# Kernel optimization log

Hardware: AMD Instinct MI355X
Metric: run time of the kernel (lower is better)

Reference implementation:

```python
import jax, jax.numpy as jnp
import numpy as np

D_K = 128

def setup_inputs() -> dict:
    key = jax.random.key(0)
    k1, k2, k3 = jax.random.split(key, 3)
    q = jax.random.normal(k1, (8192, D_K), dtype=jnp.float32)
    k = jax.random.normal(k2, (8192, D_K), dtype=jnp.float32)
    v = jax.random.normal(k3, (8192, D_K), dtype=jnp.float32)
    return {"q": q, "k": k, "v": v}

def reference(q, k, v):
    # scores: [S_q, S_k]
    scores = jnp.einsum('qd,kd->qk', q, k) / jnp.sqrt(jnp.float32(D_K))
    attn = jax.nn.softmax(scores, axis=-1)  # softmax over keys (torch default last dim)
    return jnp.einsum('qk,kd->qd', attn, v)
```

## Files before the change

### kernel.cpp

```cpp
#include <hip/hip_runtime.h>
#include <math.h>


typedef _Float16 f16x8 __attribute__((ext_vector_type(8)));
typedef float    f32x16 __attribute__((ext_vector_type(16)));

constexpr int S_LEN = 8192;
constexpr int D_K   = 128;
constexpr int NSLICE = 8;
constexpr int ITERS2 = (S_LEN / NSLICE) / 64;

constexpr size_t WS_L_OFF = 0;
constexpr size_t KV_OFF   = 262144;
constexpr size_t PART_OFF = KV_OFF + (size_t)256 * 16384;
constexpr size_t WS_NEED  = PART_OFF + (size_t)7 * S_LEN * D_K * 4;

#define CSCALE (0.08838834764831845f * 1.44269504088896340736f)

union UH8 { _Float16 h[8]; uint4 q; f16x8 v; };
union UF4 { unsigned u[4]; uint4 q; f16x8 v; };

__device__ inline void async16(const uint4* g, uint4* l) {
  __builtin_amdgcn_global_load_lds(
      (const __attribute__((address_space(1))) unsigned int*)g,
      (__attribute__((address_space(3))) unsigned int*)l, 16, 0, 0);
}

template <bool ZOUT>
__global__ __launch_bounds__(512) void attn_prep(const float* __restrict__ K,
                                                 const float* __restrict__ V,
                                                 float* __restrict__ out,
                                                 char* __restrict__ ws) {
  const int t = blockIdx.x * 512 + threadIdx.x;
  uint4* KVg = (uint4*)(ws + KV_OFF);
  if (t < 131072) {
    int kt = t >> 9, idx = t & 511;
    int lane = idx & 63, s = idx >> 6;
    int key = kt * 32 + (lane & 31);
    int d0  = s * 16 + (lane >> 5) * 8;
    const float4* src = (const float4*)(K + (size_t)key * D_K + d0);
    float4 a = src[0], b = src[1];
    float f[8] = {a.x, a.y, a.z, a.w, b.x, b.y, b.z, b.w};
    UH8 h;
    #pragma unroll
    for (int j = 0; j < 8; ++j) h.h[j] = (_Float16)f[j];
    KVg[(size_t)kt * 1024 + idx] = h.q;
  } else if (t < 262144) {
    int g = t - 131072;
    int kt = g >> 9, idx = g & 511;
    int lane = idx & 63, c = (idx >> 6) & 3, kstep = idx >> 8;
    int d  = c * 32 + (lane & 31);
    int kb = kt * 32 + kstep * 16 + (lane >> 5) * 8;
    UH8 h;
    #pragma unroll
    for (int j = 0; j < 8; ++j) h.h[j] = (_Float16)V[(size_t)(kb + j) * D_K + d];
    KVg[(size_t)kt * 1024 + 512 + idx] = h.q;
  } else if (ZOUT && t < 327680) {
    int i = t - 262144;
    float4 z = make_float4(0.f, 0.f, 0.f, 0.f);
    float4* o4 = (float4*)out;
    #pragma unroll
    for (int j = 0; j < 4; ++j) o4[(size_t)i * 4 + j] = z;
  } else if (ZOUT && t < 329728) {
    int i = t - 327680;
    ((float4*)(ws + WS_L_OFF))[i] = make_float4(0.f, 0.f, 0.f, 0.f);
  }
}

template <bool PARTIAL>
__global__ __launch_bounds__(256, 2)
void attn_main(const float* __restrict__ Qg, float* __restrict__ out,
               char* __restrict__ ws) {
  __shared__ uint4 KV[2][2048];

  const int tid   = threadIdx.x;
  const int wave  = tid >> 6;
  const int lane  = tid & 63;
  const int lrow  = lane & 31;
  const int lhalf = lane >> 5;

  const int blk = blockIdx.x;
  const int ks  = blk & 7;
  const int qb  = blk >> 3;
  const int qw  = qb * 128 + wave * 32;

  float* ws_l = (float*)(ws + WS_L_OFF);

  f16x8 qf[8];
  {
    const int q = qw + lrow;
    #pragma unroll
    for (int s = 0; s < 8; ++s) {
      const float4* src = (const float4*)(Qg + (size_t)q * D_K + s * 16 + lhalf * 8);
      float4 a = src[0], b = src[1];
      float f[8] = {a.x, a.y, a.z, a.w, b.x, b.y, b.z, b.w};
      UH8 h;
      #pragma unroll
      for (int j = 0; j < 8; ++j) h.h[j] = (_Float16)(f[j] * CSCALE);
      qf[s] = h.v;
    }
  }

  f32x16 O0{}, O1{}, O2{}, O3{};
  float lsum = 0.f;

  const uint4* KVg = (const uint4*)(ws + KV_OFF);

  {
    const size_t base = (size_t)ks * 32768;
    #pragma unroll
    for (int i = 0; i < 8; ++i)
      async16(KVg + base + i * 256 + tid, &KV[0][i * 256 + tid]);
  }

  for (int it = 0; it < ITERS2; ++it) {
    const int buf = it & 1;
    __syncthreads();

    if (it + 1 < ITERS2) {
      const size_t base = (size_t)ks * 32768 + (size_t)(it + 1) * 2048;
      #pragma unroll
      for (int i = 0; i < 8; ++i)
        async16(KVg + base + i * 256 + tid, &KV[buf ^ 1][i * 256 + tid]);
    }

    const uint4* sub0 = &KV[buf][0];
    const uint4* sub1 = &KV[buf][1024];

    f32x16 Sa0{}, Sb0{}, Sa1{}, Sb1{};
    #pragma unroll
    for (int s = 0; s < 4; ++s) {
      f16x8 ka0 = __builtin_bit_cast(f16x8, sub0[(2 * s    ) * 64 + lane]);
      f16x8 kb0 = __builtin_bit_cast(f16x8, sub0[(2 * s + 1) * 64 + lane]);
      Sa0 = __builtin_amdgcn_mfma_f32_32x32x16_f16(ka0, qf[2 * s    ], Sa0, 0, 0, 0);
      Sb0 = __builtin_amdgcn_mfma_f32_32x32x16_f16(kb0, qf[2 * s + 1], Sb0, 0, 0, 0);
    }
    #pragma unroll
    for (int s = 0; s < 4; ++s) {
      f16x8 ka1 = __builtin_bit_cast(f16x8, sub1[(2 * s    ) * 64 + lane]);
      f16x8 kb1 = __builtin_bit_cast(f16x8, sub1[(2 * s + 1) * 64 + lane]);
      Sa1 = __builtin_amdgcn_mfma_f32_32x32x16_f16(ka1, qf[2 * s    ], Sa1, 0, 0, 0);
      Sb1 = __builtin_amdgcn_mfma_f32_32x32x16_f16(kb1, qf[2 * s + 1], Sb1, 0, 0, 0);
    }

    UF4 A00, A01;
    {
      unsigned pk[8];
      #pragma unroll
      for (int i = 0; i < 8; ++i) {
        float p0 = __builtin_amdgcn_exp2f(Sa0[2 * i]     + Sb0[2 * i]);
        float p1 = __builtin_amdgcn_exp2f(Sa0[2 * i + 1] + Sb0[2 * i + 1]);
        lsum += p0 + p1;
        pk[i] = __builtin_bit_cast(unsigned, __builtin_amdgcn_cvt_pkrtz(p0, p1));
      }
      unsigned s0 = __shfl_xor(pk[0], 32), s1 = __shfl_xor(pk[1], 32);
      unsigned s2 = __shfl_xor(pk[2], 32), s3 = __shfl_xor(pk[3], 32);
      unsigned s4 = __shfl_xor(pk[4], 32), s5 = __shfl_xor(pk[5], 32);
      unsigned s6 = __shfl_xor(pk[6], 32), s7 = __shfl_xor(pk[7], 32);
      A00.u[0] = lhalf ? s2 : pk[0];
      A00.u[1] = lhalf ? s3 : pk[1];
      A00.u[2] = lhalf ? pk[2] : s0;
      A00.u[3] = lhalf ? pk[3] : s1;
      A01.u[0] = lhalf ? s6 : pk[4];
      A01.u[1] = lhalf ? s7 : pk[5];
      A01.u[2] = lhalf ? pk[6] : s4;
      A01.u[3] = lhalf ? pk[7] : s5;
    }

    #pragma unroll
    for (int kstep = 0; kstep < 2; ++kstep) {
      f16x8 pf = kstep ? A01.v : A00.v;
      f16x8 v0 = __builtin_bit_cast(f16x8, sub0[512 + kstep * 256 +   0 + lane]);
      f16x8 v1 = __builtin_bit_cast(f16x8, sub0[512 + kstep * 256 +  64 + lane]);
      f16x8 v2 = __builtin_bit_cast(f16x8, sub0[512 + kstep * 256 + 128 + lane]);
      f16x8 v3 = __builtin_bit_cast(f16x8, sub0[512 + kstep * 256 + 192 + lane]);
      O0 = __builtin_amdgcn_mfma_f32_32x32x16_f16(pf, v0, O0, 0, 0, 0);
      O1 = __builtin_amdgcn_mfma_f32_32x32x16_f16(pf, v1, O1, 0, 0, 0);
      O2 = __builtin_amdgcn_mfma_f32_32x32x16_f16(pf, v2, O2, 0, 0, 0);
      O3 = __builtin_amdgcn_mfma_f32_32x32x16_f16(pf, v3, O3, 0, 0, 0);
    }

    UF4 A10, A11;
    {
      unsigned pk[8];
      #pragma unroll
      for (int i = 0; i < 8; ++i) {
        float p0 = __builtin_amdgcn_exp2f(Sa1[2 * i]     + Sb1[2 * i]);
        float p1 = __builtin_amdgcn_exp2f(Sa1[2 * i + 1] + Sb1[2 * i + 1]);
        lsum += p0 + p1;
        pk[i] = __builtin_bit_cast(unsigned, __builtin_amdgcn_cvt_pkrtz(p0, p1));
      }
      unsigned s0 = __shfl_xor(pk[0], 32), s1 = __shfl_xor(pk[1], 32);
      unsigned s2 = __shfl_xor(pk[2], 32), s3 = __shfl_xor(pk[3], 32);
      unsigned s4 = __shfl_xor(pk[4], 32), s5 = __shfl_xor(pk[5], 32);
      unsigned s6 = __shfl_xor(pk[6], 32), s7 = __shfl_xor(pk[7], 32);
      A10.u[0] = lhalf ? s2 : pk[0];
      A10.u[1] = lhalf ? s3 : pk[1];
      A10.u[2] = lhalf ? pk[2] : s0;
      A10.u[3] = lhalf ? pk[3] : s1;
      A11.u[0] = lhalf ? s6 : pk[4];
      A11.u[1] = lhalf ? s7 : pk[5];
      A11.u[2] = lhalf ? pk[6] : s4;
      A11.u[3] = lhalf ? pk[7] : s5;
    }

    #pragma unroll
    for (int kstep = 0; kstep < 2; ++kstep) {
      f16x8 pf = kstep ? A11.v : A10.v;
      f16x8 v0 = __builtin_bit_cast(f16x8, sub1[512 + kstep * 256 +   0 + lane]);
      f16x8 v1 = __builtin_bit_cast(f16x8, sub1[512 + kstep * 256 +  64 + lane]);
      f16x8 v2 = __builtin_bit_cast(f16x8, sub1[512 + kstep * 256 + 128 + lane]);
      f16x8 v3 = __builtin_bit_cast(f16x8, sub1[512 + kstep * 256 + 192 + lane]);
      O0 = __builtin_amdgcn_mfma_f32_32x32x16_f16(pf, v0, O0, 0, 0, 0);
      O1 = __builtin_amdgcn_mfma_f32_32x32x16_f16(pf, v1, O1, 0, 0, 0);
      O2 = __builtin_amdgcn_mfma_f32_32x32x16_f16(pf, v2, O2, 0, 0, 0);
      O3 = __builtin_amdgcn_mfma_f32_32x32x16_f16(pf, v3, O3, 0, 0, 0);
    }
  }

  lsum += __shfl_xor(lsum, 32);

  if (PARTIAL) {
    if (lhalf == 0) ws_l[ks * S_LEN + qw + lrow] = lsum;
    float* obase = (ks == 0) ? out
                 : (float*)(ws + PART_OFF) + (size_t)(ks - 1) * S_LEN * D_K;
    #pragma unroll
    for (int r = 0; r < 16; ++r) {
      int row = (r & 3) + 8 * (r >> 2) + 4 * lhalf;
      float* dst = obase + (size_t)(qw + row) * D_K + lrow;
      dst[ 0] = O0[r];
      dst[32] = O1[r];
      dst[64] = O2[r];
      dst[96] = O3[r];
    }
  } else {
    if (lhalf == 0) atomicAdd(ws_l + qw + lrow, lsum);
    #pragma unroll
    for (int r = 0; r < 16; ++r) {
      int row = (r & 3) + 8 * (r >> 2) + 4 * lhalf;
      float* dst = out + (size_t)(qw + row) * D_K + lrow;
      atomicAdd(dst +  0, O0[r]);
      atomicAdd(dst + 32, O1[r]);
      atomicAdd(dst + 64, O2[r]);
      atomicAdd(dst + 96, O3[r]);
    }
  }
}

__global__ __launch_bounds__(256) void attn_norm(float* __restrict__ out,
                                                 const float* __restrict__ lpart,
                                                 const float* __restrict__ opart,
                                                 int nparts) {
  int i = blockIdx.x * 256 + threadIdx.x;
  int q = i >> 5;
  float4* o4 = (float4*)out;
  float4 acc = o4[i];
  float l = lpart[q];
  for (int s = 1; s <= nparts; ++s) {
    float4 p = ((const float4*)opart)[(size_t)(s - 1) * 262144 + i];
    acc.x += p.x; acc.y += p.y; acc.z += p.z; acc.w += p.w;
    l += lpart[s * S_LEN + q];
  }
  float inv = 1.0f / l;
  acc.x *= inv; acc.y *= inv; acc.z *= inv; acc.w *= inv;
  o4[i] = acc;
}

extern "C" void kernel_launch(void* const* d_in, const int* in_sizes, int n_in,
                              void* d_out, int out_size, void* d_ws, size_t ws_size,
                              hipStream_t stream) {
  const float* q = (const float*)d_in[0];
  const float* k = (const float*)d_in[1];
  const float* v = (const float*)d_in[2];
  float* out = (float*)d_out;
  char* ws = (char*)d_ws;

  if (ws_size >= WS_NEED) {
    attn_prep<false><<<dim3(512), dim3(512), 0, stream>>>(k, v, out, ws);
    attn_main<true><<<dim3(512), dim3(256), 0, stream>>>(q, out, ws);
    attn_norm<<<dim3(1024), dim3(256), 0, stream>>>(
        out, (const float*)(ws + WS_L_OFF), (const float*)(ws + PART_OFF), 7);
  } else {
    attn_prep<true><<<dim3(645), dim3(512), 0, stream>>>(k, v, out, ws);
    attn_main<false><<<dim3(512), dim3(256), 0, stream>>>(q, out, ws);
    attn_norm<<<dim3(1024), dim3(256), 0, stream>>>(
        out, (const float*)(ws + WS_L_OFF), (const float*)(ws + PART_OFF), 0);
  }
}
```

Baseline: 115.5 us.

## Process two 32-row query tiles per wave to reuse K/V register fragments

Each wave now handles 64 query rows (two 32-row tiles) instead of 32, so blocks shrink to 2 waves of 128 threads. K and V fragments are loaded from LDS once per sub-tile and reused for both query tiles, halving LDS read traffic per unit of MFMA work. The cost is roughly double the accumulator and Q registers per wave, plus fewer waves per block (launch bounds 128,1), which may cut occupancy and latency hiding.

```diff
diff --git a/kernel.cpp b/kernel.cpp
--- a/kernel.cpp
+++ b/kernel.cpp
@@ -67,8 +67,44 @@
   }
 }
 
+__device__ inline void softmax32(const f32x16& Sa, const f32x16& Sb, int lhalf,
+                                 float& lsum, UF4& A0, UF4& A1) {
+  unsigned pk[8];
+  #pragma unroll
+  for (int i = 0; i < 8; ++i) {
+    float p0 = __builtin_amdgcn_exp2f(Sa[2 * i]     + Sb[2 * i]);
+    float p1 = __builtin_amdgcn_exp2f(Sa[2 * i + 1] + Sb[2 * i + 1]);
+    lsum += p0 + p1;
+    pk[i] = __builtin_bit_cast(unsigned, __builtin_amdgcn_cvt_pkrtz(p0, p1));
+  }
+  unsigned s0 = __shfl_xor(pk[0], 32), s1 = __shfl_xor(pk[1], 32);
+  unsigned s2 = __shfl_xor(pk[2], 32), s3 = __shfl_xor(pk[3], 32);
+  unsigned s4 = __shfl_xor(pk[4], 32), s5 = __shfl_xor(pk[5], 32);
+  unsigned s6 = __shfl_xor(pk[6], 32), s7 = __shfl_xor(pk[7], 32);
+  A0.u[0] = lhalf ? s2 : pk[0];
+  A0.u[1] = lhalf ? s3 : pk[1];
+  A0.u[2] = lhalf ? pk[2] : s0;
+  A0.u[3] = lhalf ? pk[3] : s1;
+  A1.u[0] = lhalf ? s6 : pk[4];
+  A1.u[1] = lhalf ? s7 : pk[5];
+  A1.u[2] = lhalf ? pk[6] : s4;
+  A1.u[3] = lhalf ? pk[7] : s5;
+}
+
+__device__ inline void pv8(const UF4& A0, const UF4& A1, const f16x8* vf,
+                           f32x16* O) {
+  #pragma unroll
+  for (int kstep = 0; kstep < 2; ++kstep) {
+    f16x8 pf = kstep ? A1.v : A0.v;
+    O[0] = __builtin_amdgcn_mfma_f32_32x32x16_f16(pf, vf[kstep * 4 + 0], O[0], 0, 0, 0);
+    O[1] = __builtin_amdgcn_mfma_f32_32x32x16_f16(pf, vf[kstep * 4 + 1], O[1], 0, 0, 0);
+    O[2] = __builtin_amdgcn_mfma_f32_32x32x16_f16(pf, vf[kstep * 4 + 2], O[2], 0, 0, 0);
+    O[3] = __builtin_amdgcn_mfma_f32_32x32x16_f16(pf, vf[kstep * 4 + 3], O[3], 0, 0, 0);
+  }
+}
+
 template <bool PARTIAL>
-__global__ __launch_bounds__(256, 2)
+__global__ __launch_bounds__(128, 1)
 void attn_main(const float* __restrict__ Qg, float* __restrict__ out,
                char* __restrict__ ws) {
   __shared__ uint4 KV[2][2048];
@@ -82,13 +118,14 @@
   const int blk = blockIdx.x;
   const int ks  = blk & 7;
   const int qb  = blk >> 3;
-  const int qw  = qb * 128 + wave * 32;
+  const int qw  = qb * 128 + wave * 64;
 
   float* ws_l = (float*)(ws + WS_L_OFF);
 
-  f16x8 qf[8];
-  {
-    const int q = qw + lrow;
+  f16x8 qf[2][8];
+  #pragma unroll
+  for (int qt = 0; qt < 2; ++qt) {
+    const int q = qw + qt * 32 + lrow;
     #pragma unroll
     for (int s = 0; s < 8; ++s) {
       const float4* src = (const float4*)(Qg + (size_t)q * D_K + s * 16 + lhalf * 8);
@@ -97,20 +134,21 @@
       UH8 h;
       #pragma unroll
       for (int j = 0; j < 8; ++j) h.h[j] = (_Float16)(f[j] * CSCALE);
-      qf[s] = h.v;
-    }
-  }
-
-  f32x16 O0{}, O1{}, O2{}, O3{};
-  float lsum = 0.f;
+      qf[qt][s] = h.v;
+    }
+  }
+
+  f32x16 O0[4] = {f32x16{}, f32x16{}, f32x16{}, f32x16{}};
+  f32x16 O1[4] = {f32x16{}, f32x16{}, f32x16{}, f32x16{}};
+  float ls0 = 0.f, ls1 = 0.f;
 
   const uint4* KVg = (const uint4*)(ws + KV_OFF);
 
   {
     const size_t base = (size_t)ks * 32768;
     #pragma unroll
-    for (int i = 0; i < 8; ++i)
-      async16(KVg + base + i * 256 + tid, &KV[0][i * 256 + tid]);
+    for (int i = 0; i < 16; ++i)
+      async16(KVg + base + i * 128 + tid, &KV[0][i * 128 + tid]);
   }
 
   for (int it = 0; it < ITERS2; ++it) {
@@ -120,129 +158,88 @@
     if (it + 1 < ITERS2) {
       const size_t base = (size_t)ks * 32768 + (size_t)(it + 1) * 2048;
       #pragma unroll
+      for (int i = 0; i < 16; ++i)
+        async16(KVg + base + i * 128 + tid, &KV[buf ^ 1][i * 128 + tid]);
+    }
+
+    #pragma unroll
+    for (int st = 0; st < 2; ++st) {
+      const uint4* sub = &KV[buf][st * 1024];
+
+      f16x8 kf[8];
+      #pragma unroll
+      for (int s = 0; s < 8; ++s)
+        kf[s] = __builtin_bit_cast(f16x8, sub[s * 64 + lane]);
+
+      f32x16 Sa0{}, Sb0{}, Sa1{}, Sb1{};
+      #pragma unroll
+      for (int s = 0; s < 4; ++s) {
+        Sa0 = __builtin_amdgcn_mfma_f32_32x32x16_f16(kf[2 * s    ], qf[0][2 * s    ], Sa0, 0, 0, 0);
+        Sb0 = __builtin_amdgcn_mfma_f32_32x32x16_f16(kf[2 * s + 1], qf[0][2 * s + 1], Sb0, 0, 0, 0);
+      }
+      #pragma unroll
+      for (int s = 0; s < 4; ++s) {
+        Sa1 = __builtin_amdgcn_mfma_f32_32x32x16_f16(kf[2 * s    ], qf[1][2 * s    ], Sa1, 0, 0, 0);
+        Sb1 = __builtin_amdgcn_mfma_f32_32x32x16_f16(kf[2 * s + 1], qf[1][2 * s + 1], Sb1, 0, 0, 0);
+      }
+
+      f16x8 vf[8];
+      #pragma unroll
       for (int i = 0; i < 8; ++i)
-        async16(KVg + base + i * 256 + tid, &KV[buf ^ 1][i * 256 + tid]);
-    }
-
-    const uint4* sub0 = &KV[buf][0];
-    const uint4* sub1 = &KV[buf][1024];
-
-    f32x16 Sa0{}, Sb0{}, Sa1{}, Sb1{};
-    #pragma unroll
-    for (int s = 0; s < 4; ++s) {
-      f16x8 ka0 = __builtin_bit_cast(f16x8, sub0[(2 * s    ) * 64 + lane]);
-      f16x8 kb0 = __builtin_bit_cast(f16x8, sub0[(2 * s + 1) * 64 + lane]);
-      Sa0 = __builtin_amdgcn_mfma_f32_32x32x16_f16(ka0, qf[2 * s    ], Sa0, 0, 0, 0);
-      Sb0 = __builtin_amdgcn_mfma_f32_32x32x16_f16(kb0, qf[2 * s + 1], Sb0, 0, 0, 0);
-    }
-    #pragma unroll
-    for (int s = 0; s < 4; ++s) {
-      f16x8 ka1 = __builtin_bit_cast(f16x8, sub1[(2 * s    ) * 64 + lane]);
-      f16x8 kb1 = __builtin_bit_cast(f16x8, sub1[(2 * s + 1) * 64 + lane]);
-      Sa1 = __builtin_amdgcn_mfma_f32_32x32x16_f16(ka1, qf[2 * s    ], Sa1, 0, 0, 0);
-      Sb1 = __builtin_amdgcn_mfma_f32_32x32x16_f16(kb1, qf[2 * s + 1], Sb1, 0, 0, 0);
-    }
-
-    UF4 A00, A01;
-    {
-      unsigned pk[8];
-      #pragma unroll
-      for (int i = 0; i < 8; ++i) {
-        float p0 = __builtin_amdgcn_exp2f(Sa0[2 * i]     + Sb0[2 * i]);
-        float p1 = __builtin_amdgcn_exp2f(Sa0[2 * i + 1] + Sb0[2 * i + 1]);
-        lsum += p0 + p1;
-        pk[i] = __builtin_bit_cast(unsigned, __builtin_amdgcn_cvt_pkrtz(p0, p1));
-      }
-      unsigned s0 = __shfl_xor(pk[0], 32), s1 = __shfl_xor(pk[1], 32);
-      unsigned s2 = __shfl_xor(pk[2], 32), s3 = __shfl_xor(pk[3], 32);
-      unsigned s4 = __shfl_xor(pk[4], 32), s5 = __shfl_xor(pk[5], 32);
-      unsigned s6 = __shfl_xor(pk[6], 32), s7 = __shfl_xor(pk[7], 32);
-      A00.u[0] = lhalf ? s2 : pk[0];
-      A00.u[1] = lhalf ? s3 : pk[1];
-      A00.u[2] = lhalf ? pk[2] : s0;
-      A00.u[3] = lhalf ? pk[3] : s1;
-      A01.u[0] = lhalf ? s6 : pk[4];
-      A01.u[1] = lhalf ? s7 : pk[5];
-      A01.u[2] = lhalf ? pk[6] : s4;
-      A01.u[3] = lhalf ? pk[7] : s5;
-    }
-
-    #pragma unroll
-    for (int kstep = 0; kstep < 2; ++kstep) {
-      f16x8 pf = kstep ? A01.v : A00.v;
-      f16x8 v0 = __builtin_bit_cast(f16x8, sub0[512 + kstep * 256 +   0 + lane]);
-      f16x8 v1 = __builtin_bit_cast(f16x8, sub0[512 + kstep * 256 +  64 + lane]);
-      f16x8 v2 = __builtin_bit_cast(f16x8, sub0[512 + kstep * 256 + 128 + lane]);
-      f16x8 v3 = __builtin_bit_cast(f16x8, sub0[512 + kstep * 256 + 192 + lane]);
-      O0 = __builtin_amdgcn_mfma_f32_32x32x16_f16(pf, v0, O0, 0, 0, 0);
-      O1 = __builtin_amdgcn_mfma_f32_32x32x16_f16(pf, v1, O1, 0, 0, 0);
-      O2 = __builtin_amdgcn_mfma_f32_32x32x16_f16(pf, v2, O2, 0, 0, 0);
-      O3 = __builtin_amdgcn_mfma_f32_32x32x16_f16(pf, v3, O3, 0, 0, 0);
-    }
-
-    UF4 A10, A11;
-    {
-      unsigned pk[8];
-      #pragma unroll
-      for (int i = 0; i < 8; ++i) {
-        float p0 = __builtin_amdgcn_exp2f(Sa1[2 * i]     + Sb1[2 * i]);
-        float p1 = __builtin_amdgcn_exp2f(Sa1[2 * i + 1] + Sb1[2 * i + 1]);
-        lsum += p0 + p1;
-        pk[i] = __builtin_bit_cast(unsigned, __builtin_amdgcn_cvt_pkrtz(p0, p1));
-      }
-      unsigned s0 = __shfl_xor(pk[0], 32), s1 = __shfl_xor(pk[1], 32);
-      unsigned s2 = __shfl_xor(pk[2], 32), s3 = __shfl_xor(pk[3], 32);
-      unsigned s4 = __shfl_xor(pk[4], 32), s5 = __shfl_xor(pk[5], 32);
-      unsigned s6 = __shfl_xor(pk[6], 32), s7 = __shfl_xor(pk[7], 32);
-      A10.u[0] = lhalf ? s2 : pk[0];
-      A10.u[1] = lhalf ? s3 : pk[1];
-      A10.u[2] = lhalf ? pk[2] : s0;
-      A10.u[3] = lhalf ? pk[3] : s1;
-      A11.u[0] = lhalf ? s6 : pk[4];
-      A11.u[1] = lhalf ? s7 : pk[5];
-      A11.u[2] = lhalf ? pk[6] : s4;
-      A11.u[3] = lhalf ? pk[7] : s5;
-    }
-
-    #pragma unroll
-    for (int kstep = 0; kstep < 2; ++kstep) {
-      f16x8 pf = kstep ? A11.v : A10.v;
-      f16x8 v0 = __builtin_bit_cast(f16x8, sub1[512 + kstep * 256 +   0 + lane]);
-      f16x8 v1 = __builtin_bit_cast(f16x8, sub1[512 + kstep * 256 +  64 + lane]);
-      f16x8 v2 = __builtin_bit_cast(f16x8, sub1[512 + kstep * 256 + 128 + lane]);
-      f16x8 v3 = __builtin_bit_cast(f16x8, sub1[512 + kstep * 256 + 192 + lane]);
-      O0 = __builtin_amdgcn_mfma_f32_32x32x16_f16(pf, v0, O0, 0, 0, 0);
-      O1 = __builtin_amdgcn_mfma_f32_32x32x16_f16(pf, v1, O1, 0, 0, 0);
-      O2 = __builtin_amdgcn_mfma_f32_32x32x16_f16(pf, v2, O2, 0, 0, 0);
-      O3 = __builtin_amdgcn_mfma_f32_32x32x16_f16(pf, v3, O3, 0, 0, 0);
-    }
-  }
-
-  lsum += __shfl_xor(lsum, 32);
+        vf[i] = __builtin_bit_cast(f16x8, sub[512 + i * 64 + lane]);
+
+      UF4 A00, A01;
+      softmax32(Sa0, Sb0, lhalf, ls0, A00, A01);
+      pv8(A00, A01, vf, O0);
+
+      UF4 A10, A11;
+      softmax32(Sa1, Sb1, lhalf, ls1, A10, A11);
+      pv8(A10, A11, vf, O1);
+    }
+  }
+
+  ls0 += __shfl_xor(ls0, 32);
+  ls1 += __shfl_xor(ls1, 32);
 
   if (PARTIAL) {
-    if (lhalf == 0) ws_l[ks * S_LEN + qw + lrow] = lsum;
+    if (lhalf == 0) {
+      ws_l[ks * S_LEN + qw      + lrow] = ls0;
+      ws_l[ks * S_LEN + qw + 32 + lrow] = ls1;
+    }
     float* obase = (ks == 0) ? out
                  : (float*)(ws + PART_OFF) + (size_t)(ks - 1) * S_LEN * D_K;
     #pragma unroll
     for (int r = 0; r < 16; ++r) {
       int row = (r & 3) + 8 * (r >> 2) + 4 * lhalf;
       float* dst = obase + (size_t)(qw + row) * D_K + lrow;
-      dst[ 0] = O0[r];
-      dst[32] = O1[r];
-      dst[64] = O2[r];
-      dst[96] = O3[r];
+      dst[ 0] = O0[0][r];
+      dst[32] = O0[1][r];
+      dst[64] = O0[2][r];
+      dst[96] = O0[3][r];
+      float* dst1 = obase + (size_t)(qw + 32 + row) * D_K + lrow;
+      dst1[ 0] = O1[0][r];
+      dst1[32] = O1[1][r];
+      dst1[64] = O1[2][r];
+      dst1[96] = O1[3][r];
     }
   } else {
-    if (lhalf == 0) atomicAdd(ws_l + qw + lrow, lsum);
+    if (lhalf == 0) {
+      atomicAdd(ws_l + qw      + lrow, ls0);
+      atomicAdd(ws_l + qw + 32 + lrow, ls1);
+    }
     #pragma unroll
     for (int r = 0; r < 16; ++r) {
       int row = (r & 3) + 8 * (r >> 2) + 4 * lhalf;
       float* dst = out + (size_t)(qw + row) * D_K + lrow;
-      atomicAdd(dst +  0, O0[r]);
-      atomicAdd(dst + 32, O1[r]);
-      atomicAdd(dst + 64, O2[r]);
-      atomicAdd(dst + 96, O3[r]);
+      atomicAdd(dst +  0, O0[0][r]);
+      atomicAdd(dst + 32, O0[1][r]);
+      atomicAdd(dst + 64, O0[2][r]);
+      atomicAdd(dst + 96, O0[3][r]);
+      float* dst1 = out + (size_t)(qw + 32 + row) * D_K + lrow;
+      atomicAdd(dst1 +  0, O1[0][r]);
+      atomicAdd(dst1 + 32, O1[1][r]);
+      atomicAdd(dst1 + 64, O1[2][r]);
+      atomicAdd(dst1 + 96, O1[3][r]);
     }
   }
 }
@@ -277,12 +274,12 @@
 
   if (ws_size >= WS_NEED) {
     attn_prep<false><<<dim3(512), dim3(512), 0, stream>>>(k, v, out, ws);
-    attn_main<true><<<dim3(512), dim3(256), 0, stream>>>(q, out, ws);
+    attn_main<true><<<dim3(512), dim3(128), 0, stream>>>(q, out, ws);
     attn_norm<<<dim3(1024), dim3(256), 0, stream>>>(
         out, (const float*)(ws + WS_L_OFF), (const float*)(ws + PART_OFF), 7);
   } else {
     attn_prep<true><<<dim3(645), dim3(512), 0, stream>>>(k, v, out, ws);
-    attn_main<false><<<dim3(512), dim3(256), 0, stream>>>(q, out, ws);
+    attn_main<false><<<dim3(512), dim3(128), 0, stream>>>(q, out, ws);
     attn_norm<<<dim3(1024), dim3(256), 0, stream>>>(
         out, (const float*)(ws + WS_L_OFF), (const float*)(ws + PART_OFF), 0);
   }
```

After: 120.8 us. +4.6%, slower.

## Use permlane32_swap for P exchange, add MFMA priority and staggered block start

Applied to the files above, without the earlier changes.

Replaces the eight shfl_xor cross-half exchanges in the softmax-to-PV handoff with four permlane32_swap instructions, putting the shared code in a softmax32 helper. Raises wave priority around the MFMA blocks with s_setprio so that matrix work from one wave can overlap exp/pack work from other waves. Adds a per-block hashed s_sleep delay at kernel start to desynchronise blocks. The startup delay adds latency, and the setprio hints may or may not improve interleaving.

```diff
diff --git a/kernel.cpp b/kernel.cpp
--- a/kernel.cpp
+++ b/kernel.cpp
@@ -67,6 +67,26 @@
   }
 }
 
+__device__ inline void softmax32(const f32x16& Sa, const f32x16& Sb,
+                                 float& lsum, UF4& A0, UF4& A1) {
+  unsigned pk[8];
+  #pragma unroll
+  for (int i = 0; i < 8; ++i) {
+    float p0 = __builtin_amdgcn_exp2f(Sa[2 * i]     + Sb[2 * i]);
+    float p1 = __builtin_amdgcn_exp2f(Sa[2 * i + 1] + Sb[2 * i + 1]);
+    lsum += p0 + p1;
+    pk[i] = __builtin_bit_cast(unsigned, __builtin_amdgcn_cvt_pkrtz(p0, p1));
+  }
+  auto r0 = __builtin_amdgcn_permlane32_swap((int)pk[0], (int)pk[2], false, false);
+  auto r1 = __builtin_amdgcn_permlane32_swap((int)pk[1], (int)pk[3], false, false);
+  auto r2 = __builtin_amdgcn_permlane32_swap((int)pk[4], (int)pk[6], false, false);
+  auto r3 = __builtin_amdgcn_permlane32_swap((int)pk[5], (int)pk[7], false, false);
+  A0.u[0] = (unsigned)r0[0]; A0.u[2] = (unsigned)r0[1];
+  A0.u[1] = (unsigned)r1[0]; A0.u[3] = (unsigned)r1[1];
+  A1.u[0] = (unsigned)r2[0]; A1.u[2] = (unsigned)r2[1];
+  A1.u[1] = (unsigned)r3[0]; A1.u[3] = (unsigned)r3[1];
+}
+
 template <bool PARTIAL>
 __global__ __launch_bounds__(256, 2)
 void attn_main(const float* __restrict__ Qg, float* __restrict__ out,
@@ -83,6 +103,11 @@
   const int ks  = blk & 7;
   const int qb  = blk >> 3;
   const int qw  = qb * 128 + wave * 32;
+
+  {
+    const int delay = (int)(((unsigned)blk * 2654435761u) >> 28);
+    for (int i = 0; i < delay; ++i) __builtin_amdgcn_s_sleep(2);
+  }
 
   float* ws_l = (float*)(ws + WS_L_OFF);
 
@@ -128,6 +153,7 @@
     const uint4* sub1 = &KV[buf][1024];
 
     f32x16 Sa0{}, Sb0{}, Sa1{}, Sb1{};
+    __builtin_amdgcn_s_setprio(1);
     #pragma unroll
     for (int s = 0; s < 4; ++s) {
       f16x8 ka0 = __builtin_bit_cast(f16x8, sub0[(2 * s    ) * 64 + lane]);
@@ -142,31 +168,12 @@
       Sa1 = __builtin_amdgcn_mfma_f32_32x32x16_f16(ka1, qf[2 * s    ], Sa1, 0, 0, 0);
       Sb1 = __builtin_amdgcn_mfma_f32_32x32x16_f16(kb1, qf[2 * s + 1], Sb1, 0, 0, 0);
     }
+    __builtin_amdgcn_s_setprio(0);
 
     UF4 A00, A01;
-    {
-      unsigned pk[8];
-      #pragma unroll
-      for (int i = 0; i < 8; ++i) {
-        float p0 = __builtin_amdgcn_exp2f(Sa0[2 * i]     + Sb0[2 * i]);
-        float p1 = __builtin_amdgcn_exp2f(Sa0[2 * i + 1] + Sb0[2 * i + 1]);
-        lsum += p0 + p1;
-        pk[i] = __builtin_bit_cast(unsigned, __builtin_amdgcn_cvt_pkrtz(p0, p1));
-      }
-      unsigned s0 = __shfl_xor(pk[0], 32), s1 = __shfl_xor(pk[1], 32);
-      unsigned s2 = __shfl_xor(pk[2], 32), s3 = __shfl_xor(pk[3], 32);
-      unsigned s4 = __shfl_xor(pk[4], 32), s5 = __shfl_xor(pk[5], 32);
-      unsigned s6 = __shfl_xor(pk[6], 32), s7 = __shfl_xor(pk[7], 32);
-      A00.u[0] = lhalf ? s2 : pk[0];
-      A00.u[1] = lhalf ? s3 : pk[1];
-      A00.u[2] = lhalf ? pk[2] : s0;
-      A00.u[3] = lhalf ? pk[3] : s1;
-      A01.u[0] = lhalf ? s6 : pk[4];
-      A01.u[1] = lhalf ? s7 : pk[5];
-      A01.u[2] = lhalf ? pk[6] : s4;
-      A01.u[3] = lhalf ? pk[7] : s5;
-    }
-
+    softmax32(Sa0, Sb0, lsum, A00, A01);
+
+    __builtin_amdgcn_s_setprio(1);
     #pragma unroll
     for (int kstep = 0; kstep < 2; ++kstep) {
       f16x8 pf = kstep ? A01.v : A00.v;
@@ -179,31 +186,12 @@
       O2 = __builtin_amdgcn_mfma_f32_32x32x16_f16(pf, v2, O2, 0, 0, 0);
       O3 = __builtin_amdgcn_mfma_f32_32x32x16_f16(pf, v3, O3, 0, 0, 0);
     }
+    __builtin_amdgcn_s_setprio(0);
 
     UF4 A10, A11;
-    {
-      unsigned pk[8];
-      #pragma unroll
-      for (int i = 0; i < 8; ++i) {
-        float p0 = __builtin_amdgcn_exp2f(Sa1[2 * i]     + Sb1[2 * i]);
-        float p1 = __builtin_amdgcn_exp2f(Sa1[2 * i + 1] + Sb1[2 * i + 1]);
-        lsum += p0 + p1;
-        pk[i] = __builtin_bit_cast(unsigned, __builtin_amdgcn_cvt_pkrtz(p0, p1));
-      }
-      unsigned s0 = __shfl_xor(pk[0], 32), s1 = __shfl_xor(pk[1], 32);
-      unsigned s2 = __shfl_xor(pk[2], 32), s3 = __shfl_xor(pk[3], 32);
-      unsigned s4 = __shfl_xor(pk[4], 32), s5 = __shfl_xor(pk[5], 32);
-      unsigned s6 = __shfl_xor(pk[6], 32), s7 = __shfl_xor(pk[7], 32);
-      A10.u[0] = lhalf ? s2 : pk[0];
-      A10.u[1] = lhalf ? s3 : pk[1];
-      A10.u[2] = lhalf ? pk[2] : s0;
-      A10.u[3] = lhalf ? pk[3] : s1;
-      A11.u[0] = lhalf ? s6 : pk[4];
-      A11.u[1] = lhalf ? s7 : pk[5];
-      A11.u[2] = lhalf ? pk[6] : s4;
-      A11.u[3] = lhalf ? pk[7] : s5;
-    }
-
+    softmax32(Sa1, Sb1, lsum, A10, A11);
+
+    __builtin_amdgcn_s_setprio(1);
     #pragma unroll
     for (int kstep = 0; kstep < 2; ++kstep) {
       f16x8 pf = kstep ? A11.v : A10.v;
@@ -216,6 +204,7 @@
       O2 = __builtin_amdgcn_mfma_f32_32x32x16_f16(pf, v2, O2, 0, 0, 0);
       O3 = __builtin_amdgcn_mfma_f32_32x32x16_f16(pf, v3, O3, 0, 0, 0);
     }
+    __builtin_amdgcn_s_setprio(0);
   }
 
   lsum += __shfl_xor(lsum, 32);
```

Result: faster. 112.3 us (-2.8%).
